# Performance work log

Measured on AMD Instinct MI355X. Metric: run time of the kernel, lower is better.

The kernel has to match this reference:

```python
import jax, jax.numpy as jnp
import numpy as np

N = 8192
E = 262144
D_IN = 256
D_OUT = 256
EPS = 1e-05


def setup_inputs() -> dict:
    key = jax.random.key(0)
    kx, ke0, ke1, kw = jax.random.split(key, 4)
    x = jax.random.normal(kx, (N, D_IN), dtype=jnp.float32)
    edge_index = jnp.stack([
        jax.random.randint(ke0, (E,), 0, N, dtype=jnp.int64),
        jax.random.randint(ke1, (E,), 0, N, dtype=jnp.int64),
    ], axis=0)
    # nn.Linear(in, out, bias=False): weight shape [out, in], kaiming-uniform-ish init
    bound = 1.0 / np.sqrt(D_IN)
    W = jax.random.uniform(kw, (D_OUT, D_IN), dtype=jnp.float32, minval=-bound, maxval=bound)
    return {"x": x, "edge_index": edge_index, "W": W}


def reference(x, edge_index, W):
    n = x.shape[0]
    # A_hat = I with edges set to 1 (set semantics; duplicates harmless)
    A_hat = jnp.eye(n, dtype=x.dtype).at[edge_index[0], edge_index[1]].set(1.0)
    # D_hat = diag(1/sqrt(rowsum + eps)); A_norm = D_hat @ A_hat @ D_hat
    d_inv = 1.0 / jnp.sqrt(A_hat.sum(axis=1) + EPS)  # [N]
    A_norm = d_inv[:, None] * A_hat * d_inv[None, :]  # [N, N]
    h = x @ W.T  # [N, D_OUT]
    return jax.nn.relu(A_norm @ h)
```

## Files before the change

kernel.cpp:

```cpp
#include <hip/hip_runtime.h>
#include <hip/hip_bf16.h>
#include <math.h>

#define N_NODES 8192
#define DIM 256
#define WPR 256
#define MAXD 128
#define EPS 1e-5f

typedef __attribute__((ext_vector_type(8))) short bf16x8;
typedef __attribute__((ext_vector_type(4))) float f32x4;

__global__ __launch_bounds__(256) void scatter_all(const int* __restrict__ erows,
                                                   const int* __restrict__ ecols,
                                                   unsigned* __restrict__ bitmap,
                                                   int* __restrict__ degree,
                                                   int* __restrict__ cols, int E) {
    int t = blockIdx.x * 256 + threadIdx.x;
    int r, c;
    if (t < E) {
        r = erows[t];
        c = ecols[t];
    } else if (t < E + N_NODES) {
        r = t - E;
        c = r;
    } else {
        return;
    }
    unsigned bit = 1u << (c & 31);
    unsigned old = atomicOr(&bitmap[(size_t)r * WPR + (c >> 5)], bit);
    if (!(old & bit)) {
        int p = atomicAdd(&degree[r], 1);
        cols[(size_t)r * MAXD + p] = c;
    }
}

__device__ inline bf16x8 pack8(float4 lo, float4 hi) {
    union { __hip_bfloat16 h[8]; bf16x8 v; } u;
    u.h[0] = __float2bfloat16(lo.x); u.h[1] = __float2bfloat16(lo.y);
    u.h[2] = __float2bfloat16(lo.z); u.h[3] = __float2bfloat16(lo.w);
    u.h[4] = __float2bfloat16(hi.x); u.h[5] = __float2bfloat16(hi.y);
    u.h[6] = __float2bfloat16(hi.z); u.h[7] = __float2bfloat16(hi.w);
    return u.v;
}

__global__ __launch_bounds__(256) void gemm_fused(const float* __restrict__ x,
                                                  const float* __restrict__ W,
                                                  const int* __restrict__ degree,
                                                  __hip_bfloat16* __restrict__ g) {
    int wave = threadIdx.x >> 6;
    int lane = threadIdx.x & 63;
    int bm = blockIdx.x * 64 + wave * 16;
    int bn = blockIdx.y * 64;
    int quad = lane >> 4;
    int l16 = lane & 15;
    f32x4 acc[4] = {};
    const float* arow = x + (size_t)(bm + l16) * DIM + quad * 8;
#pragma unroll
    for (int k0 = 0; k0 < DIM; k0 += 32) {
        float4 a0 = *(const float4*)(arow + k0);
        float4 a1 = *(const float4*)(arow + k0 + 4);
        bf16x8 a = pack8(a0, a1);
#pragma unroll
        for (int s = 0; s < 4; s++) {
            const float* brow = W + (size_t)(bn + s * 16 + l16) * DIM + quad * 8 + k0;
            float4 b0 = *(const float4*)(brow);
            float4 b1 = *(const float4*)(brow + 4);
            bf16x8 b = pack8(b0, b1);
            acc[s] = __builtin_amdgcn_mfma_f32_16x16x32_bf16(a, b, acc[s], 0, 0, 0);
        }
    }
#pragma unroll
    for (int r = 0; r < 4; r++) {
        int m = bm + quad * 4 + r;
        float s0 = rsqrtf((float)degree[m] + EPS);
#pragma unroll
        for (int s = 0; s < 4; s++)
            g[(size_t)m * DIM + bn + s * 16 + l16] = __float2bfloat16(s0 * acc[s][r]);
    }
}

__global__ __launch_bounds__(256) void aggregate(const int* __restrict__ degree,
                                                 const int* __restrict__ cols,
                                                 const uint2* __restrict__ g2,
                                                 float* __restrict__ out) {
    int wave = threadIdx.x >> 6;
    int lane = threadIdx.x & 63;
    int row = blockIdx.x * 4 + wave;
    int n = degree[row];
    const int* cl = cols + (size_t)row * MAXD;
    float a0[4] = {0.f, 0.f, 0.f, 0.f};
    float a1[4] = {0.f, 0.f, 0.f, 0.f};
    float a2[4] = {0.f, 0.f, 0.f, 0.f};
    float a3[4] = {0.f, 0.f, 0.f, 0.f};
    int i = 0;
    for (; i + 4 <= n; i += 4) {
        int4 j4 = *(const int4*)(cl + i);
        uint2 u0 = g2[(size_t)j4.x * 64 + lane];
        uint2 u1 = g2[(size_t)j4.y * 64 + lane];
        uint2 u2 = g2[(size_t)j4.z * 64 + lane];
        uint2 u3 = g2[(size_t)j4.w * 64 + lane];
        a0[0] += __uint_as_float(u0.x << 16); a0[1] += __uint_as_float(u0.x & 0xffff0000u);
        a0[2] += __uint_as_float(u0.y << 16); a0[3] += __uint_as_float(u0.y & 0xffff0000u);
        a1[0] += __uint_as_float(u1.x << 16); a1[1] += __uint_as_float(u1.x & 0xffff0000u);
        a1[2] += __uint_as_float(u1.y << 16); a1[3] += __uint_as_float(u1.y & 0xffff0000u);
        a2[0] += __uint_as_float(u2.x << 16); a2[1] += __uint_as_float(u2.x & 0xffff0000u);
        a2[2] += __uint_as_float(u2.y << 16); a2[3] += __uint_as_float(u2.y & 0xffff0000u);
        a3[0] += __uint_as_float(u3.x << 16); a3[1] += __uint_as_float(u3.x & 0xffff0000u);
        a3[2] += __uint_as_float(u3.y << 16); a3[3] += __uint_as_float(u3.y & 0xffff0000u);
    }
    for (; i < n; i++) {
        uint2 u = g2[(size_t)cl[i] * 64 + lane];
        a0[0] += __uint_as_float(u.x << 16); a0[1] += __uint_as_float(u.x & 0xffff0000u);
        a0[2] += __uint_as_float(u.y << 16); a0[3] += __uint_as_float(u.y & 0xffff0000u);
    }
    float s = rsqrtf((float)n + EPS);
    float4 o;
    o.x = fmaxf(s * ((a0[0] + a1[0]) + (a2[0] + a3[0])), 0.f);
    o.y = fmaxf(s * ((a0[1] + a1[1]) + (a2[1] + a3[1])), 0.f);
    o.z = fmaxf(s * ((a0[2] + a1[2]) + (a2[2] + a3[2])), 0.f);
    o.w = fmaxf(s * ((a0[3] + a1[3]) + (a2[3] + a3[3])), 0.f);
    *(float4*)(out + (size_t)row * DIM + lane * 4) = o;
}

extern "C" void kernel_launch(void* const* d_in, const int* in_sizes, int n_in,
                              void* d_out, int out_size, void* d_ws, size_t ws_size,
                              hipStream_t stream) {
    const float* x = (const float*)d_in[0];
    const int* ei = (const int*)d_in[1];
    const float* W = (const float*)d_in[2];
    float* out = (float*)d_out;
    int E = in_sizes[1] / 2;

    unsigned char* ws = (unsigned char*)d_ws;
    size_t off = 0;
    unsigned* bitmap = (unsigned*)(ws + off); off += (size_t)N_NODES * WPR * 4;
    int* degree = (int*)(ws + off);           off += (size_t)N_NODES * 4;
    int* cols = (int*)(ws + off);             off += (size_t)N_NODES * MAXD * 4;
    __hip_bfloat16* g = (__hip_bfloat16*)(ws + off); off += (size_t)N_NODES * DIM * 2;

    hipMemsetAsync(bitmap, 0, (size_t)N_NODES * WPR * 4 + (size_t)N_NODES * 4, stream);
    int total = E + N_NODES;
    scatter_all<<<(total + 255) / 256, 256, 0, stream>>>(ei, ei + E, bitmap, degree, cols, E);
    dim3 ggrid(N_NODES / 64, DIM / 64);
    gemm_fused<<<ggrid, 256, 0, stream>>>(x, W, degree, g);
    aggregate<<<N_NODES / 4, 256, 0, stream>>>(degree, cols, (const uint2*)g, out);
}
```

Measured before the change: 123.5 us.

## Fuse memset, scatter, GEMM and aggregation into one cooperative persistent kernel

Replaces the memset and three separate kernel launches with a single cooperative kernel of 512 blocks that zeroes the bitmap, builds the adjacency lists, computes the bf16 GEMM and aggregates, separating the phases with grid-wide syncs. This removes launch overheads and inter-kernel gaps. The aggregation loop is also widened to eight independent accumulators to keep more gathers in flight. In exchange it adds three grid barriers and limits parallelism to the resident grid, with each wave handling several rows in the aggregation phase.

```diff
diff --git a/kernel.cpp b/kernel.cpp
--- a/kernel.cpp
+++ b/kernel.cpp
@@ -1,39 +1,21 @@
 #include <hip/hip_runtime.h>
+#include <hip/hip_cooperative_groups.h>
 #include <hip/hip_bf16.h>
 #include <math.h>
+
+namespace cg = cooperative_groups;
 
 #define N_NODES 8192
 #define DIM 256
 #define WPR 256
 #define MAXD 128
 #define EPS 1e-5f
+#define NBLK 512
+#define NTHR 256
+#define NTHREADS (NBLK * NTHR)
 
 typedef __attribute__((ext_vector_type(8))) short bf16x8;
 typedef __attribute__((ext_vector_type(4))) float f32x4;
-
-__global__ __launch_bounds__(256) void scatter_all(const int* __restrict__ erows,
-                                                   const int* __restrict__ ecols,
-                                                   unsigned* __restrict__ bitmap,
-                                                   int* __restrict__ degree,
-                                                   int* __restrict__ cols, int E) {
-    int t = blockIdx.x * 256 + threadIdx.x;
-    int r, c;
-    if (t < E) {
-        r = erows[t];
-        c = ecols[t];
-    } else if (t < E + N_NODES) {
-        r = t - E;
-        c = r;
-    } else {
-        return;
-    }
-    unsigned bit = 1u << (c & 31);
-    unsigned old = atomicOr(&bitmap[(size_t)r * WPR + (c >> 5)], bit);
-    if (!(old & bit)) {
-        int p = atomicAdd(&degree[r], 1);
-        cols[(size_t)r * MAXD + p] = c;
-    }
-}
 
 __device__ inline bf16x8 pack8(float4 lo, float4 hi) {
     union { __hip_bfloat16 h[8]; bf16x8 v; } u;
@@ -44,83 +26,134 @@
     return u.v;
 }
 
-__global__ __launch_bounds__(256) void gemm_fused(const float* __restrict__ x,
-                                                  const float* __restrict__ W,
-                                                  const int* __restrict__ degree,
-                                                  __hip_bfloat16* __restrict__ g) {
-    int wave = threadIdx.x >> 6;
-    int lane = threadIdx.x & 63;
-    int bm = blockIdx.x * 64 + wave * 16;
-    int bn = blockIdx.y * 64;
-    int quad = lane >> 4;
-    int l16 = lane & 15;
-    f32x4 acc[4] = {};
-    const float* arow = x + (size_t)(bm + l16) * DIM + quad * 8;
-#pragma unroll
-    for (int k0 = 0; k0 < DIM; k0 += 32) {
-        float4 a0 = *(const float4*)(arow + k0);
-        float4 a1 = *(const float4*)(arow + k0 + 4);
-        bf16x8 a = pack8(a0, a1);
-#pragma unroll
-        for (int s = 0; s < 4; s++) {
-            const float* brow = W + (size_t)(bn + s * 16 + l16) * DIM + quad * 8 + k0;
-            float4 b0 = *(const float4*)(brow);
-            float4 b1 = *(const float4*)(brow + 4);
-            bf16x8 b = pack8(b0, b1);
-            acc[s] = __builtin_amdgcn_mfma_f32_16x16x32_bf16(a, b, acc[s], 0, 0, 0);
+__device__ inline float bfhi(unsigned u) { return __uint_as_float(u & 0xffff0000u); }
+__device__ inline float bflo(unsigned u) { return __uint_as_float(u << 16); }
+
+__global__ __launch_bounds__(NTHR, 2) void gcn_fused(
+    const float* __restrict__ x,
+    const int* __restrict__ erows, const int* __restrict__ ecols,
+    const float* __restrict__ W, float* __restrict__ out,
+    unsigned* __restrict__ bitmap, int* __restrict__ degree,
+    int* __restrict__ cols, __hip_bfloat16* __restrict__ g, int E) {
+
+    cg::grid_group grid = cg::this_grid();
+    const int tid = blockIdx.x * NTHR + threadIdx.x;
+
+    {
+        uint4 z = make_uint4(0, 0, 0, 0);
+        uint4* zb = (uint4*)bitmap;
+        const int nv = (N_NODES * WPR + N_NODES) / 4;
+        for (int i = tid; i < nv; i += NTHREADS) zb[i] = z;
+    }
+    __threadfence();
+    grid.sync();
+
+    {
+        const int total = E + N_NODES;
+        for (int t = tid; t < total; t += NTHREADS) {
+            int r, c;
+            if (t < E) { r = erows[t]; c = ecols[t]; }
+            else       { r = t - E;   c = r; }
+            unsigned bit = 1u << (c & 31);
+            unsigned old = atomicOr(&bitmap[(size_t)r * WPR + (c >> 5)], bit);
+            if (!(old & bit)) {
+                int p = atomicAdd(&degree[r], 1);
+                cols[(size_t)r * MAXD + p] = c;
+            }
         }
     }
+    __threadfence();
+    grid.sync();
+
+    {
+        int wave = threadIdx.x >> 6;
+        int lane = threadIdx.x & 63;
+        int bm = (blockIdx.x >> 2) * 64 + wave * 16;
+        int bn = (blockIdx.x & 3) * 64;
+        int quad = lane >> 4;
+        int l16 = lane & 15;
+        f32x4 acc[4] = {};
+        const float* arow = x + (size_t)(bm + l16) * DIM + quad * 8;
 #pragma unroll
-    for (int r = 0; r < 4; r++) {
-        int m = bm + quad * 4 + r;
-        float s0 = rsqrtf((float)degree[m] + EPS);
+        for (int k0 = 0; k0 < DIM; k0 += 32) {
+            float4 a0 = *(const float4*)(arow + k0);
+            float4 a1 = *(const float4*)(arow + k0 + 4);
+            bf16x8 a = pack8(a0, a1);
 #pragma unroll
-        for (int s = 0; s < 4; s++)
-            g[(size_t)m * DIM + bn + s * 16 + l16] = __float2bfloat16(s0 * acc[s][r]);
+            for (int s = 0; s < 4; s++) {
+                const float* brow = W + (size_t)(bn + s * 16 + l16) * DIM + quad * 8 + k0;
+                bf16x8 b = pack8(*(const float4*)(brow), *(const float4*)(brow + 4));
+                acc[s] = __builtin_amdgcn_mfma_f32_16x16x32_bf16(a, b, acc[s], 0, 0, 0);
+            }
+        }
+#pragma unroll
+        for (int r = 0; r < 4; r++) {
+            int m = bm + quad * 4 + r;
+            float s0 = rsqrtf((float)degree[m] + EPS);
+#pragma unroll
+            for (int s = 0; s < 4; s++)
+                g[(size_t)m * DIM + bn + s * 16 + l16] = __float2bfloat16(s0 * acc[s][r]);
+        }
     }
-}
+    __threadfence();
+    grid.sync();
 
-__global__ __launch_bounds__(256) void aggregate(const int* __restrict__ degree,
-                                                 const int* __restrict__ cols,
-                                                 const uint2* __restrict__ g2,
-                                                 float* __restrict__ out) {
-    int wave = threadIdx.x >> 6;
-    int lane = threadIdx.x & 63;
-    int row = blockIdx.x * 4 + wave;
-    int n = degree[row];
-    const int* cl = cols + (size_t)row * MAXD;
-    float a0[4] = {0.f, 0.f, 0.f, 0.f};
-    float a1[4] = {0.f, 0.f, 0.f, 0.f};
-    float a2[4] = {0.f, 0.f, 0.f, 0.f};
-    float a3[4] = {0.f, 0.f, 0.f, 0.f};
-    int i = 0;
-    for (; i + 4 <= n; i += 4) {
-        int4 j4 = *(const int4*)(cl + i);
-        uint2 u0 = g2[(size_t)j4.x * 64 + lane];
-        uint2 u1 = g2[(size_t)j4.y * 64 + lane];
-        uint2 u2 = g2[(size_t)j4.z * 64 + lane];
-        uint2 u3 = g2[(size_t)j4.w * 64 + lane];
-        a0[0] += __uint_as_float(u0.x << 16); a0[1] += __uint_as_float(u0.x & 0xffff0000u);
-        a0[2] += __uint_as_float(u0.y << 16); a0[3] += __uint_as_float(u0.y & 0xffff0000u);
-        a1[0] += __uint_as_float(u1.x << 16); a1[1] += __uint_as_float(u1.x & 0xffff0000u);
-        a1[2] += __uint_as_float(u1.y << 16); a1[3] += __uint_as_float(u1.y & 0xffff0000u);
-        a2[0] += __uint_as_float(u2.x << 16); a2[1] += __uint_as_float(u2.x & 0xffff0000u);
-        a2[2] += __uint_as_float(u2.y << 16); a2[3] += __uint_as_float(u2.y & 0xffff0000u);
-        a3[0] += __uint_as_float(u3.x << 16); a3[1] += __uint_as_float(u3.x & 0xffff0000u);
-        a3[2] += __uint_as_float(u3.y << 16); a3[3] += __uint_as_float(u3.y & 0xffff0000u);
+    {
+        const uint2* g2 = (const uint2*)g;
+        int wid = tid >> 6;
+        int lane = tid & 63;
+        for (int row = wid; row < N_NODES; row += 2048) {
+            int n = degree[row];
+            const int* cl = cols + (size_t)row * MAXD;
+            float s0[4] = {0.f,0.f,0.f,0.f}, s1[4] = {0.f,0.f,0.f,0.f};
+            float s2[4] = {0.f,0.f,0.f,0.f}, s3[4] = {0.f,0.f,0.f,0.f};
+            float s4[4] = {0.f,0.f,0.f,0.f}, s5[4] = {0.f,0.f,0.f,0.f};
+            float s6[4] = {0.f,0.f,0.f,0.f}, s7[4] = {0.f,0.f,0.f,0.f};
+            int i = 0;
+            for (; i + 8 <= n; i += 8) {
+                int4 ja = *(const int4*)(cl + i);
+                int4 jb = *(const int4*)(cl + i + 4);
+                uint2 u0 = g2[(size_t)ja.x * 64 + lane];
+                uint2 u1 = g2[(size_t)ja.y * 64 + lane];
+                uint2 u2 = g2[(size_t)ja.z * 64 + lane];
+                uint2 u3 = g2[(size_t)ja.w * 64 + lane];
+                uint2 u4 = g2[(size_t)jb.x * 64 + lane];
+                uint2 u5 = g2[(size_t)jb.y * 64 + lane];
+                uint2 u6 = g2[(size_t)jb.z * 64 + lane];
+                uint2 u7 = g2[(size_t)jb.w * 64 + lane];
+                s0[0] += bflo(u0.x); s0[1] += bfhi(u0.x); s0[2] += bflo(u0.y); s0[3] += bfhi(u0.y);
+                s1[0] += bflo(u1.x); s1[1] += bfhi(u1.x); s1[2] += bflo(u1.y); s1[3] += bfhi(u1.y);
+                s2[0] += bflo(u2.x); s2[1] += bfhi(u2.x); s2[2] += bflo(u2.y); s2[3] += bfhi(u2.y);
+                s3[0] += bflo(u3.x); s3[1] += bfhi(u3.x); s3[2] += bflo(u3.y); s3[3] += bfhi(u3.y);
+                s4[0] += bflo(u4.x); s4[1] += bfhi(u4.x); s4[2] += bflo(u4.y); s4[3] += bfhi(u4.y);
+                s5[0] += bflo(u5.x); s5[1] += bfhi(u5.x); s5[2] += bflo(u5.y); s5[3] += bfhi(u5.y);
+                s6[0] += bflo(u6.x); s6[1] += bfhi(u6.x); s6[2] += bflo(u6.y); s6[3] += bfhi(u6.y);
+                s7[0] += bflo(u7.x); s7[1] += bfhi(u7.x); s7[2] += bflo(u7.y); s7[3] += bfhi(u7.y);
+            }
+            for (; i + 4 <= n; i += 4) {
+                int4 ja = *(const int4*)(cl + i);
+                uint2 u0 = g2[(size_t)ja.x * 64 + lane];
+                uint2 u1 = g2[(size_t)ja.y * 64 + lane];
+                uint2 u2 = g2[(size_t)ja.z * 64 + lane];
+                uint2 u3 = g2[(size_t)ja.w * 64 + lane];
+                s0[0] += bflo(u0.x); s0[1] += bfhi(u0.x); s0[2] += bflo(u0.y); s0[3] += bfhi(u0.y);
+                s1[0] += bflo(u1.x); s1[1] += bfhi(u1.x); s1[2] += bflo(u1.y); s1[3] += bfhi(u1.y);
+                s2[0] += bflo(u2.x); s2[1] += bfhi(u2.x); s2[2] += bflo(u2.y); s2[3] += bfhi(u2.y);
+                s3[0] += bflo(u3.x); s3[1] += bfhi(u3.x); s3[2] += bflo(u3.y); s3[3] += bfhi(u3.y);
+            }
+            for (; i < n; i++) {
+                uint2 u = g2[(size_t)cl[i] * 64 + lane];
+                s0[0] += bflo(u.x); s0[1] += bfhi(u.x); s0[2] += bflo(u.y); s0[3] += bfhi(u.y);
+            }
+            float sc = rsqrtf((float)n + EPS);
+            float4 o;
+            o.x = fmaxf(sc * (((s0[0]+s1[0])+(s2[0]+s3[0])) + ((s4[0]+s5[0])+(s6[0]+s7[0]))), 0.f);
+            o.y = fmaxf(sc * (((s0[1]+s1[1])+(s2[1]+s3[1])) + ((s4[1]+s5[1])+(s6[1]+s7[1]))), 0.f);
+            o.z = fmaxf(sc * (((s0[2]+s1[2])+(s2[2]+s3[2])) + ((s4[2]+s5[2])+(s6[2]+s7[2]))), 0.f);
+            o.w = fmaxf(sc * (((s0[3]+s1[3])+(s2[3]+s3[3])) + ((s4[3]+s5[3])+(s6[3]+s7[3]))), 0.f);
+            *(float4*)(out + (size_t)row * DIM + lane * 4) = o;
+        }
     }
-    for (; i < n; i++) {
-        uint2 u = g2[(size_t)cl[i] * 64 + lane];
-        a0[0] += __uint_as_float(u.x << 16); a0[1] += __uint_as_float(u.x & 0xffff0000u);
-        a0[2] += __uint_as_float(u.y << 16); a0[3] += __uint_as_float(u.y & 0xffff0000u);
-    }
-    float s = rsqrtf((float)n + EPS);
-    float4 o;
-    o.x = fmaxf(s * ((a0[0] + a1[0]) + (a2[0] + a3[0])), 0.f);
-    o.y = fmaxf(s * ((a0[1] + a1[1]) + (a2[1] + a3[1])), 0.f);
-    o.z = fmaxf(s * ((a0[2] + a1[2]) + (a2[2] + a3[2])), 0.f);
-    o.w = fmaxf(s * ((a0[3] + a1[3]) + (a2[3] + a3[3])), 0.f);
-    *(float4*)(out + (size_t)row * DIM + lane * 4) = o;
 }
 
 extern "C" void kernel_launch(void* const* d_in, const int* in_sizes, int n_in,
@@ -139,10 +172,9 @@
     int* cols = (int*)(ws + off);             off += (size_t)N_NODES * MAXD * 4;
     __hip_bfloat16* g = (__hip_bfloat16*)(ws + off); off += (size_t)N_NODES * DIM * 2;
 
-    hipMemsetAsync(bitmap, 0, (size_t)N_NODES * WPR * 4 + (size_t)N_NODES * 4, stream);
-    int total = E + N_NODES;
-    scatter_all<<<(total + 255) / 256, 256, 0, stream>>>(ei, ei + E, bitmap, degree, cols, E);
-    dim3 ggrid(N_NODES / 64, DIM / 64);
-    gemm_fused<<<ggrid, 256, 0, stream>>>(x, W, degree, g);
-    aggregate<<<N_NODES / 4, 256, 0, stream>>>(degree, cols, (const uint2*)g, out);
+    const int* erows = ei;
+    const int* ecols = ei + E;
+    void* args[] = {(void*)&x, (void*)&erows, (void*)&ecols, (void*)&W, (void*)&out,
+                    (void*)&bitmap, (void*)&degree, (void*)&cols, (void*)&g, (void*)&E};
+    hipLaunchCooperativeKernel((void*)gcn_fused, dim3(NBLK), dim3(NTHR), args, 0, stream);
 }
```

After: 439.6 us. 256% more time.
